# Kernel tuning notes

Hardware: AMD Instinct MI355X
Metric: run time of the kernel (lower is better)

The kernel has to match this reference:

```python
import jax, jax.numpy as jnp
import numpy as np

B, S, D, H = 4, 1024, 1024, 16
DEPTH = D // H


def setup_inputs() -> dict:
    key = jax.random.key(0)
    ks = jax.random.split(key, 12)
    scale = 1.0 / np.sqrt(D)
    return {
        "query": jax.random.normal(ks[0], (B, S, D), jnp.float32),
        "key_in": jax.random.normal(ks[1], (B, S, D), jnp.float32),
        "value": jax.random.normal(ks[2], (B, S, D), jnp.float32),
        "mask": jnp.zeros((B, 1, 1, S), jnp.float32),
        "wq": jax.random.normal(ks[3], (D, D), jnp.float32) * scale,
        "bq": jnp.zeros((D,), jnp.float32),
        "wk": jax.random.normal(ks[4], (D, D), jnp.float32) * scale,
        "bk": jnp.zeros((D,), jnp.float32),
        "wv": jax.random.normal(ks[5], (D, D), jnp.float32) * scale,
        "bv": jnp.zeros((D,), jnp.float32),
        "wo": jax.random.normal(ks[6], (D, D), jnp.float32) * scale,
        "bo": jnp.zeros((D,), jnp.float32),
    }


def _split_heads(x):
    b, s, _ = x.shape
    return x.reshape(b, s, H, DEPTH).transpose(0, 2, 1, 3)  # [B,H,S,depth]


def reference(query, key_in, value, mask, wq, bq, wk, bk, wv, bv, wo, bo):
    q = _split_heads(query @ wq + bq)
    k = _split_heads(key_in @ wk + bk)
    v = _split_heads(value @ wv + bv)
    # scaled dot-product attention, full O(S^2) scores as in the original
    scores = jnp.einsum("bhqd,bhkd->bhqk", q, k) / jnp.sqrt(jnp.float32(DEPTH))
    scores = scores + mask * (-1e9)
    attn = jax.nn.softmax(scores, axis=-1)
    ctx = jnp.einsum("bhqk,bhkd->bhqd", attn, v)
    concat = ctx.transpose(0, 2, 1, 3).reshape(query.shape[0], -1, D)
    return concat @ wo + bo
```

## Files before the change

### kernel.cpp

```cpp
#include <hip/hip_runtime.h>
#include <hip/hip_bf16.h>
#include <stdint.h>

#define B_ 4
#define S_ 1024
#define D_ 1024
#define H_ 16
#define DEPTH_ 64

typedef __attribute__((ext_vector_type(8))) short bf16x8;
typedef __attribute__((ext_vector_type(4))) float f32x4;
typedef unsigned short ubf16;

__device__ __forceinline__ ubf16 f2bf(float f) {
  union { float f; unsigned u; } v; v.f = f;
  unsigned r = v.u + 0x7fffu + ((v.u >> 16) & 1u);
  return (ubf16)(r >> 16);
}

__device__ __forceinline__ void async16(void* lds, const void* g) {
  __builtin_amdgcn_global_load_lds(
      (const __attribute__((address_space(1))) void*)g,
      (__attribute__((address_space(3))) void*)lds, 16, 0, 0);
}

struct Cvt3 { const float* src[3]; ubf16* dst[3]; };
__global__ __launch_bounds__(256) void convert3_bf16(Cvt3 a, int n4) {
  int i = blockIdx.x * 256 + threadIdx.x;
  const float* src = a.src[blockIdx.y];
  ubf16* dst = a.dst[blockIdx.y];
  if (i < n4) {
    float4 v = ((const float4*)src)[i];
    ushort4 o;
    o.x = f2bf(v.x); o.y = f2bf(v.y); o.z = f2bf(v.z); o.w = f2bf(v.w);
    ((ushort4*)dst)[i] = o;
  }
}

struct Tp4 { const float* W[4]; ubf16* WT[4]; };
__global__ __launch_bounds__(256) void transpose4_bf16(Tp4 a) {
  __shared__ float tile[32][33];
  const float* W = a.W[blockIdx.z];
  ubf16* WT = a.WT[blockIdx.z];
  int n0 = blockIdx.x * 32, k0 = blockIdx.y * 32;
  int tx = threadIdx.x & 31, ty = threadIdx.x >> 5;
#pragma unroll
  for (int i = 0; i < 4; ++i)
    tile[ty + i * 8][tx] = W[(size_t)(k0 + ty + i * 8) * D_ + n0 + tx];
  __syncthreads();
#pragma unroll
  for (int i = 0; i < 4; ++i)
    WT[(size_t)(n0 + ty + i * 8) * D_ + k0 + tx] = f2bf(tile[tx][ty + i * 8]);
}

struct GemmUnit {
  const ubf16* A; const ubf16* BT; const float* bias; void* out; int mode;
};
struct GemmArgs { GemmUnit u[3]; };

__global__ __launch_bounds__(256) void gemm_bt(GemmArgs args, int M, int N, int K) {
  const GemmUnit gu = args.u[blockIdx.z];
  const int orig = blockIdx.x + (blockIdx.y << 3);
  const int xcd = orig & 7, j = orig >> 3;
  const int bm0 = (xcd * 4 + (j & 3)) * 128;
  const int bn0 = (j >> 2) * 128;
  const int tid = threadIdx.x, wid = tid >> 6, lane = tid & 63;
  const int wr = wid >> 1, wc = wid & 1;
  const int l15 = lane & 15, l4 = lane >> 4;
  __shared__ __align__(16) ubf16 As[128 * 32];
  __shared__ __align__(16) ubf16 Bs[128 * 32];
  f32x4 acc[4][4] = {};

  for (int kt = 0; kt < K; kt += 32) {
#pragma unroll
    for (int i = 0; i < 2; ++i) {
      int c = i * 256 + tid;
      int r = c >> 2, ch = c & 3;
      async16((char*)As + i * 4096 + wid * 1024,
              gu.A + (size_t)(bm0 + r) * K + kt + ch * 8);
      async16((char*)Bs + i * 4096 + wid * 1024,
              gu.BT + (size_t)(bn0 + r) * K + kt + ch * 8);
    }
    __syncthreads();
    bf16x8 af[4], bfr[4];
#pragma unroll
    for (int mi = 0; mi < 4; ++mi)
      af[mi] = *(const bf16x8*)&As[(wr * 64 + mi * 16 + l15) * 32 + l4 * 8];
#pragma unroll
    for (int ni = 0; ni < 4; ++ni)
      bfr[ni] = *(const bf16x8*)&Bs[(wc * 64 + ni * 16 + l15) * 32 + l4 * 8];
#pragma unroll
    for (int mi = 0; mi < 4; ++mi)
#pragma unroll
      for (int ni = 0; ni < 4; ++ni)
        acc[mi][ni] = __builtin_amdgcn_mfma_f32_16x16x32_bf16(af[mi], bfr[ni], acc[mi][ni], 0, 0, 0);
    __syncthreads();
  }

  float bv[4];
#pragma unroll
  for (int ni = 0; ni < 4; ++ni) bv[ni] = gu.bias[bn0 + wc * 64 + ni * 16 + l15];
#pragma unroll
  for (int mi = 0; mi < 4; ++mi) {
#pragma unroll
    for (int ni = 0; ni < 4; ++ni) {
#pragma unroll
      for (int r = 0; r < 4; ++r) {
        int m = bm0 + wr * 64 + mi * 16 + l4 * 4 + r;
        int n = bn0 + wc * 64 + ni * 16 + l15;
        float v = acc[mi][ni][r] + bv[ni];
        if (gu.mode == 0) {
          ((ubf16*)gu.out)[(size_t)m * N + n] = f2bf(v);
        } else if (gu.mode == 1) {
          int b = m >> 10, s = m & 1023, h = n >> 6, d = n & 63;
          ((ubf16*)gu.out)[(((size_t)(b * H_ + h)) * DEPTH_ + d) * S_ + s] = f2bf(v);
        } else {
          ((float*)gu.out)[(size_t)m * N + n] = v;
        }
      }
    }
  }
}

__global__ __launch_bounds__(256) void attention_fwd(
    const ubf16* __restrict__ Q, const ubf16* __restrict__ Kg,
    const ubf16* __restrict__ VT, const float* __restrict__ mask,
    ubf16* __restrict__ ctx) {
  const int lid = blockIdx.y * 8 + blockIdx.x;
  const int t0 = (lid & 7) * 64 + (lid >> 3);
  const int qt = t0 & 7, bh = t0 >> 3;
  const int b = bh >> 4, h = bh & 15;
  const int tid = threadIdx.x, wid = tid >> 6, lane = tid & 63;
  const int l15 = lane & 15, l4 = lane >> 4;
  const int q0 = qt * 128 + wid * 32;

  __shared__ __align__(16) ubf16 Ks[2][4096];
  __shared__ __align__(16) ubf16 Vs[2][4096];
  __shared__ __align__(16) ubf16 Ps[4][32][72];

  const ubf16* kb = Kg + ((size_t)(b * S_)) * D_ + h * DEPTH_;
  const ubf16* vb = VT + ((size_t)bh) * DEPTH_ * S_;

  bf16x8 aq[2][2];
#pragma unroll
  for (int mi = 0; mi < 2; ++mi)
#pragma unroll
    for (int kk = 0; kk < 2; ++kk)
      aq[mi][kk] = *(const bf16x8*)&Q[((size_t)(b * S_ + q0 + mi * 16 + l15)) * D_ +
                                      h * DEPTH_ + kk * 32 + l4 * 8];

  bf16x8 ones;
#pragma unroll
  for (int j = 0; j < 8; ++j) ones[j] = (short)0x3F80;

  f32x4 cacc[2][4] = {};
  f32x4 csum[2] = {};

  const float* mrow = mask + b * S_;
  const float C1 = 0.125f * 1.44269504f;
  const float CM = -1.0e9f * 1.44269504f;

  auto stage = [&](int bf, int kt) {
#pragma unroll
    for (int i = 0; i < 2; ++i) {
      int c = i * 256 + tid;
      int r = c >> 3, cg = (c & 7) ^ (r & 7);
      async16((char*)&Ks[bf][0] + i * 4096 + wid * 1024,
              kb + (size_t)(kt + r) * D_ + cg * 8);
      async16((char*)&Vs[bf][0] + i * 4096 + wid * 1024,
              vb + (size_t)r * S_ + kt + cg * 8);
    }
  };

  stage(0, 0);
  __syncthreads();

  for (int t = 0; t < 16; ++t) {
    const int cur = t & 1;
    const int kt = t * 64;
    if (t < 15) stage(cur ^ 1, kt + 64);

    bf16x8 kf[4][2];
#pragma unroll
    for (int nf = 0; nf < 4; ++nf)
#pragma unroll
      for (int kk = 0; kk < 2; ++kk) {
        int kr = nf * 16 + l15;
        int c16 = (kk * 4 + l4) ^ (kr & 7);
        kf[nf][kk] = *(const bf16x8*)((const char*)&Ks[cur][0] + kr * 128 + c16 * 16);
      }
    bf16x8 vf[4][2];
#pragma unroll
    for (int df = 0; df < 4; ++df)
#pragma unroll
      for (int kk = 0; kk < 2; ++kk) {
        int dr = df * 16 + l15;
        int c16 = (kk * 4 + l4) ^ (dr & 7);
        vf[df][kk] = *(const bf16x8*)((const char*)&Vs[cur][0] + dr * 128 + c16 * 16);
      }

    f32x4 sc[2][4];
#pragma unroll
    for (int mi = 0; mi < 2; ++mi)
#pragma unroll
      for (int nf = 0; nf < 4; ++nf) {
        f32x4 z = {0.f, 0.f, 0.f, 0.f};
        z = __builtin_amdgcn_mfma_f32_16x16x32_bf16(aq[mi][0], kf[nf][0], z, 0, 0, 0);
        z = __builtin_amdgcn_mfma_f32_16x16x32_bf16(aq[mi][1], kf[nf][1], z, 0, 0, 0);
        sc[mi][nf] = z;
      }

    float mvl[4];
#pragma unroll
    for (int nf = 0; nf < 4; ++nf) mvl[nf] = mrow[kt + nf * 16 + l15] * CM;

#pragma unroll
    for (int mi = 0; mi < 2; ++mi)
#pragma unroll
      for (int nf = 0; nf < 4; ++nf)
#pragma unroll
        for (int r = 0; r < 4; ++r) {
          float p = __builtin_amdgcn_exp2f(fmaf(sc[mi][nf][r], C1, mvl[nf]));
          Ps[wid][mi * 16 + l4 * 4 + r][nf * 16 + l15] = f2bf(p);
        }

    bf16x8 pf[2][2];
#pragma unroll
    for (int mi = 0; mi < 2; ++mi)
#pragma unroll
      for (int kk = 0; kk < 2; ++kk)
        pf[mi][kk] = *(const bf16x8*)&Ps[wid][mi * 16 + l15][kk * 32 + l4 * 8];

#pragma unroll
    for (int mi = 0; mi < 2; ++mi) {
#pragma unroll
      for (int df = 0; df < 4; ++df) {
        cacc[mi][df] = __builtin_amdgcn_mfma_f32_16x16x32_bf16(pf[mi][0], vf[df][0], cacc[mi][df], 0, 0, 0);
        cacc[mi][df] = __builtin_amdgcn_mfma_f32_16x16x32_bf16(pf[mi][1], vf[df][1], cacc[mi][df], 0, 0, 0);
      }
      csum[mi] = __builtin_amdgcn_mfma_f32_16x16x32_bf16(pf[mi][0], ones, csum[mi], 0, 0, 0);
      csum[mi] = __builtin_amdgcn_mfma_f32_16x16x32_bf16(pf[mi][1], ones, csum[mi], 0, 0, 0);
    }

    __syncthreads();
  }

#pragma unroll
  for (int mi = 0; mi < 2; ++mi) {
    float inv[4];
#pragma unroll
    for (int r = 0; r < 4; ++r) inv[r] = 1.0f / csum[mi][r];
#pragma unroll
    for (int df = 0; df < 4; ++df)
#pragma unroll
      for (int r = 0; r < 4; ++r) {
        int srow = q0 + mi * 16 + l4 * 4 + r;
        float v = cacc[mi][df][r] * inv[r];
        ctx[((size_t)(b * S_ + srow)) * D_ + h * DEPTH_ + df * 16 + l15] = f2bf(v);
      }
  }
}

extern "C" void kernel_launch(void* const* d_in, const int* in_sizes, int n_in,
                              void* d_out, int out_size, void* d_ws, size_t ws_size,
                              hipStream_t stream) {
  const float* query  = (const float*)d_in[0];
  const float* key_in = (const float*)d_in[1];
  const float* value  = (const float*)d_in[2];
  const float* mask   = (const float*)d_in[3];
  const float* wq = (const float*)d_in[4];
  const float* bq = (const float*)d_in[5];
  const float* wk = (const float*)d_in[6];
  const float* bk = (const float*)d_in[7];
  const float* wv = (const float*)d_in[8];
  const float* bv = (const float*)d_in[9];
  const float* wo = (const float*)d_in[10];
  const float* bo = (const float*)d_in[11];

  char* ws = (char*)d_ws;
  const size_t MB = 1024 * 1024;
  ubf16* Xq  = (ubf16*)(ws + 0 * MB);
  ubf16* Xk  = (ubf16*)(ws + 8 * MB);
  ubf16* Xv  = (ubf16*)(ws + 16 * MB);
  ubf16* WqT = (ubf16*)(ws + 24 * MB);
  ubf16* WkT = (ubf16*)(ws + 26 * MB);
  ubf16* WvT = (ubf16*)(ws + 28 * MB);
  ubf16* WoT = (ubf16*)(ws + 30 * MB);
  ubf16* Qb  = (ubf16*)(ws + 32 * MB);
  ubf16* Kb  = (ubf16*)(ws + 40 * MB);
  ubf16* VTb = (ubf16*)(ws + 48 * MB);
  ubf16* Ctx = (ubf16*)(ws + 56 * MB);

  const int n4 = (B_ * S_ * D_) / 4;
  Cvt3 c3;
  c3.src[0] = query;  c3.dst[0] = Xq;
  c3.src[1] = key_in; c3.dst[1] = Xk;
  c3.src[2] = value;  c3.dst[2] = Xv;
  convert3_bf16<<<dim3((n4 + 255) / 256, 3), dim3(256), 0, stream>>>(c3, n4);

  Tp4 t4;
  t4.W[0] = wq; t4.WT[0] = WqT;
  t4.W[1] = wk; t4.WT[1] = WkT;
  t4.W[2] = wv; t4.WT[2] = WvT;
  t4.W[3] = wo; t4.WT[3] = WoT;
  transpose4_bf16<<<dim3(32, 32, 4), dim3(256), 0, stream>>>(t4);

  GemmArgs g1;
  g1.u[0] = {Xq, WqT, bq, (void*)Qb, 0};
  g1.u[1] = {Xk, WkT, bk, (void*)Kb, 0};
  g1.u[2] = {Xv, WvT, bv, (void*)VTb, 1};
  gemm_bt<<<dim3(8, 32, 3), dim3(256), 0, stream>>>(g1, 4096, 1024, 1024);

  attention_fwd<<<dim3(8, 64), dim3(256), 0, stream>>>(Qb, Kb, VTb, mask, Ctx);

  GemmArgs g2;
  g2.u[0] = {Ctx, WoT, bo, d_out, 2};
  g2.u[1] = g2.u[0];
  g2.u[2] = g2.u[0];
  gemm_bt<<<dim3(8, 32, 1), dim3(256), 0, stream>>>(g2, 4096, 1024, 1024);
}
```

Baseline: 132.8 us.

## Replace QKV projection GEMM with 256x256-tile double-buffered 8-wave kernel

Adds a new QKV projection GEMM that uses 256x256 output tiles, 512 threads (8 waves) and double-buffered LDS filled by async global-to-LDS loads. Loads for the A and B tiles are interleaved with two MFMA phases per k-step, using explicit barriers, waitcnts and setprio. A and B data now feeds more MFMAs per byte loaded, and the grid becomes 192 workgroups with an XCD-aware mapping. The trade-off is fewer workgroups than the 768 of the old launch, which may underfill the CUs, plus higher register and LDS use.

```diff
diff --git a/kernel.cpp b/kernel.cpp
--- a/kernel.cpp
+++ b/kernel.cpp
@@ -11,6 +11,8 @@
 typedef __attribute__((ext_vector_type(8))) short bf16x8;
 typedef __attribute__((ext_vector_type(4))) float f32x4;
 typedef unsigned short ubf16;
+
+#define FULL_BAR() do { asm volatile("" ::: "memory"); __builtin_amdgcn_s_barrier(); asm volatile("" ::: "memory"); } while (0)
 
 __device__ __forceinline__ ubf16 f2bf(float f) {
   union { float f; unsigned u; } v; v.f = f;
@@ -57,6 +59,104 @@
   const ubf16* A; const ubf16* BT; const float* bias; void* out; int mode;
 };
 struct GemmArgs { GemmUnit u[3]; };
+
+__global__ __launch_bounds__(512, 2) void gemm_qkv_256(GemmArgs args) {
+  const int lin = blockIdx.x;
+  const int wg = (lin & 7) * 24 + (lin >> 3);
+  const int z = wg >> 6, rr = wg & 63;
+  const GemmUnit gu = args.u[z];
+  const int bm0 = (rr >> 2) * 256, bn0 = (rr & 3) * 256;
+  const int tid = threadIdx.x, wid = tid >> 6, lane = tid & 63;
+  const int wm = wid >> 2, wn = wid & 3;
+  const int l15 = lane & 15, l4 = lane >> 4;
+
+  __shared__ __align__(16) ubf16 Ab[2][256 * 32];
+  __shared__ __align__(16) ubf16 Bb[2][256 * 32];
+
+  f32x4 acc[8][4] = {};
+
+  auto stageA = [&](int bf, int t) {
+#pragma unroll
+    for (int i = 0; i < 2; ++i) {
+      int row = i * 128 + (tid >> 2);
+      async16((char*)&Ab[bf][0] + i * 8192 + wid * 1024,
+              gu.A + (size_t)(bm0 + row) * 1024 + t * 32 + (tid & 3) * 8);
+    }
+  };
+  auto stageB = [&](int bf, int t) {
+#pragma unroll
+    for (int i = 0; i < 2; ++i) {
+      int row = i * 128 + (tid >> 2);
+      async16((char*)&Bb[bf][0] + i * 8192 + wid * 1024,
+              gu.BT + (size_t)(bn0 + row) * 1024 + t * 32 + (tid & 3) * 8);
+    }
+  };
+
+  stageA(0, 0); stageB(0, 0); stageA(1, 1);
+  asm volatile("s_waitcnt vmcnt(0)" ::: "memory");
+  FULL_BAR();
+
+  for (int u = 0; u < 32; ++u) {
+    const int cur = u & 1;
+    bf16x8 af[8], bf[2];
+#pragma unroll
+    for (int mi = 0; mi < 8; ++mi)
+      af[mi] = *(const bf16x8*)&Ab[cur][(wm * 128 + mi * 16 + l15) * 32 + l4 * 8];
+#pragma unroll
+    for (int ni = 0; ni < 2; ++ni)
+      bf[ni] = *(const bf16x8*)&Bb[cur][(wn * 64 + ni * 16 + l15) * 32 + l4 * 8];
+    if (u < 31) stageB(cur ^ 1, u + 1);
+    FULL_BAR();
+    asm volatile("s_waitcnt lgkmcnt(0)" ::: "memory");
+    __builtin_amdgcn_sched_barrier(0);
+    __builtin_amdgcn_s_setprio(1);
+#pragma unroll
+    for (int mi = 0; mi < 8; ++mi) {
+      acc[mi][0] = __builtin_amdgcn_mfma_f32_16x16x32_bf16(af[mi], bf[0], acc[mi][0], 0, 0, 0);
+      acc[mi][1] = __builtin_amdgcn_mfma_f32_16x16x32_bf16(af[mi], bf[1], acc[mi][1], 0, 0, 0);
+    }
+    __builtin_amdgcn_s_setprio(0);
+    FULL_BAR();
+    bf16x8 bg[2];
+#pragma unroll
+    for (int ni = 0; ni < 2; ++ni)
+      bg[ni] = *(const bf16x8*)&Bb[cur][(wn * 64 + (ni + 2) * 16 + l15) * 32 + l4 * 8];
+    if (u < 30) stageA(cur, u + 2);
+    FULL_BAR();
+    asm volatile("s_waitcnt lgkmcnt(0)" ::: "memory");
+    __builtin_amdgcn_sched_barrier(0);
+    __builtin_amdgcn_s_setprio(1);
+#pragma unroll
+    for (int mi = 0; mi < 8; ++mi) {
+      acc[mi][2] = __builtin_amdgcn_mfma_f32_16x16x32_bf16(af[mi], bg[0], acc[mi][2], 0, 0, 0);
+      acc[mi][3] = __builtin_amdgcn_mfma_f32_16x16x32_bf16(af[mi], bg[1], acc[mi][3], 0, 0, 0);
+    }
+    __builtin_amdgcn_s_setprio(0);
+    if (u < 30) asm volatile("s_waitcnt vmcnt(2)" ::: "memory");
+    else        asm volatile("s_waitcnt vmcnt(0)" ::: "memory");
+    FULL_BAR();
+  }
+
+  float bv[4];
+#pragma unroll
+  for (int ni = 0; ni < 4; ++ni) bv[ni] = gu.bias[bn0 + wn * 64 + ni * 16 + l15];
+#pragma unroll
+  for (int mi = 0; mi < 8; ++mi)
+#pragma unroll
+    for (int ni = 0; ni < 4; ++ni)
+#pragma unroll
+      for (int r = 0; r < 4; ++r) {
+        int m = bm0 + wm * 128 + mi * 16 + l4 * 4 + r;
+        int n = bn0 + wn * 64 + ni * 16 + l15;
+        float v = acc[mi][ni][r] + bv[ni];
+        if (gu.mode == 0) {
+          ((ubf16*)gu.out)[(size_t)m * 1024 + n] = f2bf(v);
+        } else {
+          int b = m >> 10, s = m & 1023, h = n >> 6, d = n & 63;
+          ((ubf16*)gu.out)[(((size_t)(b * H_ + h)) * DEPTH_ + d) * S_ + s] = f2bf(v);
+        }
+      }
+}
 
 __global__ __launch_bounds__(256) void gemm_bt(GemmArgs args, int M, int N, int K) {
   const GemmUnit gu = args.u[blockIdx.z];
@@ -309,7 +409,7 @@
   g1.u[0] = {Xq, WqT, bq, (void*)Qb, 0};
   g1.u[1] = {Xk, WkT, bk, (void*)Kb, 0};
   g1.u[2] = {Xv, WvT, bv, (void*)VTb, 1};
-  gemm_bt<<<dim3(8, 32, 3), dim3(256), 0, stream>>>(g1, 4096, 1024, 1024);
+  gemm_qkv_256<<<dim3(192), dim3(512), 0, stream>>>(g1);
 
   attention_fwd<<<dim3(8, 64), dim3(256), 0, stream>>>(Qb, Kb, VTb, mask, Ctx);
 
```

Measured after the change: 157.8 us. +18.8%, slower.

## Double-buffer GEMM LDS tiles with async prefetch and XOR-swizzled layout

Applied to the files above, without the earlier changes.

The projection GEMM now uses two LDS buffers. It issues the next K-tile's async global-to-LDS loads before computing on the current tile, waiting with a partial vmcnt so the loads overlap the MFMA work. Each 16-byte chunk's column is XOR-swizzled by row, to cut LDS bank conflicts on the fragment reads. K is hardcoded to 1024 so the loop count is a compile-time constant. This doubles the GEMM's shared memory use, which may lower occupancy, and it relies on hand-placed waitcnt and barrier counts being correct.

```diff
diff --git a/kernel.cpp b/kernel.cpp
--- a/kernel.cpp
+++ b/kernel.cpp
@@ -58,7 +58,7 @@
 };
 struct GemmArgs { GemmUnit u[3]; };
 
-__global__ __launch_bounds__(256) void gemm_bt(GemmArgs args, int M, int N, int K) {
+__global__ __launch_bounds__(256) void gemm_bt(GemmArgs args, int M, int N) {
   const GemmUnit gu = args.u[blockIdx.z];
   const int orig = blockIdx.x + (blockIdx.y << 3);
   const int xcd = orig & 7, j = orig >> 3;
@@ -67,34 +67,59 @@
   const int tid = threadIdx.x, wid = tid >> 6, lane = tid & 63;
   const int wr = wid >> 1, wc = wid & 1;
   const int l15 = lane & 15, l4 = lane >> 4;
-  __shared__ __align__(16) ubf16 As[128 * 32];
-  __shared__ __align__(16) ubf16 Bs[128 * 32];
+  const int K = 1024;
+
+  __shared__ __align__(16) ubf16 As[2][128 * 32];
+  __shared__ __align__(16) ubf16 Bs[2][128 * 32];
   f32x4 acc[4][4] = {};
 
-  for (int kt = 0; kt < K; kt += 32) {
+  auto stage = [&](int bf, int kt) {
 #pragma unroll
     for (int i = 0; i < 2; ++i) {
       int c = i * 256 + tid;
-      int r = c >> 2, ch = c & 3;
-      async16((char*)As + i * 4096 + wid * 1024,
-              gu.A + (size_t)(bm0 + r) * K + kt + ch * 8);
-      async16((char*)Bs + i * 4096 + wid * 1024,
-              gu.BT + (size_t)(bn0 + r) * K + kt + ch * 8);
-    }
-    __syncthreads();
+      int r = c >> 2, s = c & 3;
+      int cg = s ^ ((r >> 1) & 3);
+      async16((char*)&As[bf][0] + i * 4096 + wid * 1024,
+              gu.A + (size_t)(bm0 + r) * K + kt + cg * 8);
+      async16((char*)&Bs[bf][0] + i * 4096 + wid * 1024,
+              gu.BT + (size_t)(bn0 + r) * K + kt + cg * 8);
+    }
+  };
+
+  stage(0, 0);
+  for (int t = 0; t < 32; ++t) {
+    const int cur = t & 1;
+    if (t < 31) {
+      stage(cur ^ 1, (t + 1) * 32);
+      asm volatile("s_waitcnt vmcnt(4)" ::: "memory");
+    } else {
+      asm volatile("s_waitcnt vmcnt(0)" ::: "memory");
+    }
+    __builtin_amdgcn_s_barrier();
+    asm volatile("" ::: "memory");
+
     bf16x8 af[4], bfr[4];
 #pragma unroll
-    for (int mi = 0; mi < 4; ++mi)
-      af[mi] = *(const bf16x8*)&As[(wr * 64 + mi * 16 + l15) * 32 + l4 * 8];
-#pragma unroll
-    for (int ni = 0; ni < 4; ++ni)
-      bfr[ni] = *(const bf16x8*)&Bs[(wc * 64 + ni * 16 + l15) * 32 + l4 * 8];
+    for (int mi = 0; mi < 4; ++mi) {
+      int r = wr * 64 + mi * 16 + l15;
+      int sl = l4 ^ ((r >> 1) & 3);
+      af[mi] = *(const bf16x8*)((const char*)&As[cur][0] + r * 64 + sl * 16);
+    }
+#pragma unroll
+    for (int ni = 0; ni < 4; ++ni) {
+      int r = wc * 64 + ni * 16 + l15;
+      int sl = l4 ^ ((r >> 1) & 3);
+      bfr[ni] = *(const bf16x8*)((const char*)&Bs[cur][0] + r * 64 + sl * 16);
+    }
 #pragma unroll
     for (int mi = 0; mi < 4; ++mi)
 #pragma unroll
       for (int ni = 0; ni < 4; ++ni)
         acc[mi][ni] = __builtin_amdgcn_mfma_f32_16x16x32_bf16(af[mi], bfr[ni], acc[mi][ni], 0, 0, 0);
-    __syncthreads();
+
+    asm volatile("" ::: "memory");
+    __builtin_amdgcn_s_barrier();
+    asm volatile("" ::: "memory");
   }
 
   float bv[4];
@@ -309,7 +334,7 @@
   g1.u[0] = {Xq, WqT, bq, (void*)Qb, 0};
   g1.u[1] = {Xk, WkT, bk, (void*)Kb, 0};
   g1.u[2] = {Xv, WvT, bv, (void*)VTb, 1};
-  gemm_bt<<<dim3(8, 32, 3), dim3(256), 0, stream>>>(g1, 4096, 1024, 1024);
+  gemm_bt<<<dim3(8, 32, 3), dim3(256), 0, stream>>>(g1, 4096, 1024);
 
   attention_fwd<<<dim3(8, 64), dim3(256), 0, stream>>>(Qb, Kb, VTb, mask, Ctx);
 
@@ -317,5 +342,5 @@
   g2.u[0] = {Ctx, WoT, bo, d_out, 2};
   g2.u[1] = g2.u[0];
   g2.u[2] = g2.u[0];
-  gemm_bt<<<dim3(8, 32, 1), dim3(256), 0, stream>>>(g2, 4096, 1024, 1024);
-}
+  gemm_bt<<<dim3(8, 32, 1), dim3(256), 0, stream>>>(g2, 4096, 1024);
+}
```

Result: no change. 133.6 us (+0.6%).

## Triple-buffer GEMM LDS tiles with async prefetch and XOR-swizzled layout

Applied to the files above, without the earlier changes.

Replaces the single-buffered load/sync/compute loop in the projection GEMM with a three-stage LDS ring. Two tiles are kept in flight via global_load_lds, and manual vmcnt waits plus raw barriers control ordering. The LDS layout is XOR-swizzled per row pair to reduce bank conflicts on the fragment reads. K is now a compile-time constant. This triples LDS use per block, which may lower occupancy, and it relies on hand-counted wait counts being correct.

```diff
diff --git a/kernel.cpp b/kernel.cpp
--- a/kernel.cpp
+++ b/kernel.cpp
@@ -11,6 +11,8 @@
 typedef __attribute__((ext_vector_type(8))) short bf16x8;
 typedef __attribute__((ext_vector_type(4))) float f32x4;
 typedef unsigned short ubf16;
+
+#define BAR() do { asm volatile("" ::: "memory"); __builtin_amdgcn_s_barrier(); asm volatile("" ::: "memory"); } while (0)
 
 __device__ __forceinline__ ubf16 f2bf(float f) {
   union { float f; unsigned u; } v; v.f = f;
@@ -58,7 +60,7 @@
 };
 struct GemmArgs { GemmUnit u[3]; };
 
-__global__ __launch_bounds__(256) void gemm_bt(GemmArgs args, int M, int N, int K) {
+__global__ __launch_bounds__(256) void gemm_bt(GemmArgs args, int M, int N) {
   const GemmUnit gu = args.u[blockIdx.z];
   const int orig = blockIdx.x + (blockIdx.y << 3);
   const int xcd = orig & 7, j = orig >> 3;
@@ -67,35 +69,71 @@
   const int tid = threadIdx.x, wid = tid >> 6, lane = tid & 63;
   const int wr = wid >> 1, wc = wid & 1;
   const int l15 = lane & 15, l4 = lane >> 4;
-  __shared__ __align__(16) ubf16 As[128 * 32];
-  __shared__ __align__(16) ubf16 Bs[128 * 32];
+  const int K = 1024;
+
+  __shared__ __align__(16) ubf16 As[3][128 * 32];
+  __shared__ __align__(16) ubf16 Bs[3][128 * 32];
   f32x4 acc[4][4] = {};
 
-  for (int kt = 0; kt < K; kt += 32) {
+  const ubf16* aCur[2]; const ubf16* bCur[2];
+#pragma unroll
+  for (int i = 0; i < 2; ++i) {
+    int c = i * 256 + tid;
+    int r = c >> 2, s = c & 3;
+    int cg = s ^ ((r >> 1) & 3);
+    aCur[i] = gu.A + (size_t)(bm0 + r) * K + cg * 8;
+    bCur[i] = gu.BT + (size_t)(bn0 + r) * K + cg * 8;
+  }
+  auto stageAdv = [&](int bf) {
 #pragma unroll
     for (int i = 0; i < 2; ++i) {
-      int c = i * 256 + tid;
-      int r = c >> 2, ch = c & 3;
-      async16((char*)As + i * 4096 + wid * 1024,
-              gu.A + (size_t)(bm0 + r) * K + kt + ch * 8);
-      async16((char*)Bs + i * 4096 + wid * 1024,
-              gu.BT + (size_t)(bn0 + r) * K + kt + ch * 8);
-    }
-    __syncthreads();
+      async16((char*)&As[bf][0] + i * 4096 + wid * 1024, aCur[i]);
+      async16((char*)&Bs[bf][0] + i * 4096 + wid * 1024, bCur[i]);
+      aCur[i] += 32; bCur[i] += 32;
+    }
+  };
+  int aOff[4], bOff[4];
+#pragma unroll
+  for (int f = 0; f < 4; ++f) {
+    int ra = wr * 64 + f * 16 + l15;
+    aOff[f] = ra * 64 + (l4 ^ ((ra >> 1) & 3)) * 16;
+    int rb = wc * 64 + f * 16 + l15;
+    bOff[f] = rb * 64 + (l4 ^ ((rb >> 1) & 3)) * 16;
+  }
+  auto body = [&](int bf) {
     bf16x8 af[4], bfr[4];
 #pragma unroll
     for (int mi = 0; mi < 4; ++mi)
-      af[mi] = *(const bf16x8*)&As[(wr * 64 + mi * 16 + l15) * 32 + l4 * 8];
+      af[mi] = *(const bf16x8*)((const char*)&As[bf][0] + aOff[mi]);
 #pragma unroll
     for (int ni = 0; ni < 4; ++ni)
-      bfr[ni] = *(const bf16x8*)&Bs[(wc * 64 + ni * 16 + l15) * 32 + l4 * 8];
+      bfr[ni] = *(const bf16x8*)((const char*)&Bs[bf][0] + bOff[ni]);
 #pragma unroll
     for (int mi = 0; mi < 4; ++mi)
 #pragma unroll
       for (int ni = 0; ni < 4; ++ni)
         acc[mi][ni] = __builtin_amdgcn_mfma_f32_16x16x32_bf16(af[mi], bfr[ni], acc[mi][ni], 0, 0, 0);
-    __syncthreads();
-  }
+  };
+
+  stageAdv(0); stageAdv(1);
+#pragma unroll 1
+  for (int tt = 0; tt < 10; ++tt) {
+#pragma unroll
+    for (int u = 0; u < 3; ++u) {
+      stageAdv((u + 2) % 3);
+      asm volatile("s_waitcnt vmcnt(8)" ::: "memory");
+      BAR();
+      body(u);
+      BAR();
+    }
+  }
+  asm volatile("s_waitcnt vmcnt(4)" ::: "memory");
+  BAR();
+  body(0);
+  BAR();
+  asm volatile("s_waitcnt vmcnt(0)" ::: "memory");
+  BAR();
+  body(1);
 
   float bv[4];
 #pragma unroll
@@ -309,7 +347,7 @@
   g1.u[0] = {Xq, WqT, bq, (void*)Qb, 0};
   g1.u[1] = {Xk, WkT, bk, (void*)Kb, 0};
   g1.u[2] = {Xv, WvT, bv, (void*)VTb, 1};
-  gemm_bt<<<dim3(8, 32, 3), dim3(256), 0, stream>>>(g1, 4096, 1024, 1024);
+  gemm_bt<<<dim3(8, 32, 3), dim3(256), 0, stream>>>(g1, 4096, 1024);
 
   attention_fwd<<<dim3(8, 64), dim3(256), 0, stream>>>(Qb, Kb, VTb, mask, Ctx);
 
@@ -317,5 +355,5 @@
   g2.u[0] = {Ctx, WoT, bo, d_out, 2};
   g2.u[1] = g2.u[0];
   g2.u[2] = g2.u[0];
-  gemm_bt<<<dim3(8, 32, 1), dim3(256), 0, stream>>>(g2, 4096, 1024, 1024);
-}
+  gemm_bt<<<dim3(8, 32, 1), dim3(256), 0, stream>>>(g2, 4096, 1024);
+}
```

Result: faster. 128.9 us (-3.0%).
